# Kernel tuning notes

Hardware: AMD Instinct MI355X
Metric: run time of the kernel (lower is better)

The kernel has to match this reference:

```python
import jax, jax.numpy as jnp
import numpy as np

N_HEAD = 16
ROPE_BASE = 10000.0
EPS = 1e-6


def _rms_norm(x):
    return x / jnp.sqrt(jnp.mean(x * x, axis=-1, keepdims=True) + EPS)


def _rotary_cos_sin(n_pos, dim, dtype):
    # NOTE: faithful to the source, n_pos == n_head (not seq_len) because
    # Rotary.forward reads x.shape[2] of a (B,T,H,D) tensor.
    inv_freq = 1.0 / (ROPE_BASE ** (jnp.arange(0, dim, 2, dtype=jnp.float32) / dim))
    t = jnp.arange(n_pos, dtype=jnp.float32)
    freqs = jnp.outer(t, inv_freq)  # (n_pos, dim//2)
    return jnp.cos(freqs).astype(dtype)[None, None], jnp.sin(freqs).astype(dtype)[None, None]


def _apply_rotary(x, cos, sin):
    d = x.shape[-1] // 2
    x1, x2 = x[..., :d], x[..., d:]
    return jnp.concatenate([x1 * cos + x2 * sin, -x1 * sin + x2 * cos], axis=-1)


def setup_inputs() -> dict:
    key = jax.random.key(0)
    ks = jax.random.split(key, 8)
    B, T, C = 4, 1024, 2048
    x = jax.random.normal(ks[0], (B, T, C), dtype=jnp.float32)
    v1 = jax.random.normal(ks[1], (B, T, N_HEAD, C // N_HEAD), dtype=jnp.float32)
    s = 0.02
    W_qkv = jax.random.normal(ks[2], (C, 3 * C), dtype=jnp.float32) * s
    b_qkv = jax.random.normal(ks[3], (3 * C,), dtype=jnp.float32) * s
    W_proj = jax.random.normal(ks[4], (C, C), dtype=jnp.float32) * s
    b_proj = jax.random.normal(ks[5], (C,), dtype=jnp.float32) * s
    lamb = jnp.float32(0.5)
    return {"x": x, "v1": v1, "W_qkv": W_qkv, "b_qkv": b_qkv,
            "W_proj": W_proj, "b_proj": b_proj, "lamb": lamb}


def reference(x, v1, W_qkv, b_qkv, W_proj, b_proj, lamb):
    B, T, C = x.shape
    H = N_HEAD
    D = C // H
    qkv = x @ W_qkv + b_qkv  # (B,T,3C)
    q, k, v = jnp.split(qkv, 3, axis=-1)
    q = q.reshape(B, T, H, D)
    k = k.reshape(B, T, H, D)
    v = v.reshape(B, T, H, D)
    v1 = v1.reshape(B, T, H, D)
    value = (1.0 - lamb) * v + lamb * v1  # lambda value-residual mix
    q = _rms_norm(q)
    k = _rms_norm(k)
    cos, sin = _rotary_cos_sin(H, D, x.dtype)  # rotary over head axis (source bug, kept)
    q = _apply_rotary(q, cos, sin)
    k = _apply_rotary(k, cos, sin)
    # causal attention, default flex_attention scale 1/sqrt(D)
    scale = 1.0 / jnp.sqrt(jnp.float32(D)).astype(x.dtype)
    scores = jnp.einsum('bqhd,bkhd->bhqk', q, k) * scale
    causal = jnp.tril(jnp.ones((T, T), dtype=bool))
    scores = jnp.where(causal[None, None], scores, jnp.finfo(scores.dtype).min)
    probs = jax.nn.softmax(scores, axis=-1)
    attn = jnp.einsum('bhqk,bkhd->bqhd', probs, value).reshape(B, T, C)
    out = attn @ W_proj + b_proj
    return out, v1
```

## Files before the change

kernel.cpp:

```cpp
#include <hip/hip_runtime.h>
#include <stdint.h>
#include <stddef.h>

typedef unsigned short u16;
typedef __attribute__((ext_vector_type(8))) short  bf16x8;
typedef __attribute__((ext_vector_type(4))) unsigned short u16x4;
typedef __attribute__((ext_vector_type(4))) float  f32x4;

#define DEVI __device__ __forceinline__

DEVI float bf2f(u16 u){ union{uint32_t i; float f;} v; v.i = ((uint32_t)u)<<16; return v.f; }
DEVI u16 f2bf(float f){ union{float f; uint32_t i;} v; v.f=f; uint32_t r = v.i + 0x7fffu + ((v.i>>16)&1u); return (u16)(r>>16); }

DEVI void gload_lds16(const void* g, void* l){
  __builtin_amdgcn_global_load_lds((const __attribute__((address_space(1))) void*)g,
                                   (__attribute__((address_space(3))) void*)l, 16, 0, 0);
}

__global__ __launch_bounds__(256) void k_prep(
    const float* __restrict__ x,     u16* __restrict__ xb,
    const float* __restrict__ Wqkv,  u16* __restrict__ WqkvT,
    const float* __restrict__ Wproj, u16* __restrict__ WprojT)
{
  __shared__ float tile[32][33];
  int bid = blockIdx.x;
  int tid = threadIdx.x;
  if (bid < 2048){
    int i = (bid*256 + tid)*4;
    const int st = 2048*256*4;
    for (; i < 8388608; i += st){
      f32x4 v = *(const f32x4*)(x + i);
      u16x4 o;
      #pragma unroll
      for (int j=0;j<4;j++) o[j] = f2bf(v[j]);
      *(u16x4*)(xb + i) = o;
    }
    return;
  }
  const float* in; u16* out; int K, N, nb, kb;
  if (bid < 2048 + 12288){
    int b2 = bid - 2048; in = Wqkv; out = WqkvT; K = 2048; N = 6144;
    nb = (b2 % 192)*32; kb = (b2 / 192)*32;
  } else {
    int b3 = bid - 2048 - 12288; in = Wproj; out = WprojT; K = 2048; N = 2048;
    nb = (b3 % 64)*32; kb = (b3 / 64)*32;
  }
  int tx = tid & 31, ty = tid >> 5;
  #pragma unroll
  for (int i=0;i<32;i+=8)
    tile[ty+i][tx] = in[(size_t)(kb+ty+i)*N + nb+tx];
  __syncthreads();
  #pragma unroll
  for (int i=0;i<32;i+=8)
    out[(size_t)(nb+ty+i)*K + kb+tx] = f2bf(tile[tx][ty+i]);
}

#define STG_A(SLAB, GSRC) \
  gload_lds16((GSRC) + off0, (SLAB) + tid*8);
#define STG_B(SLAB, GSRC) \
  gload_lds16((GSRC) + off0, (SLAB) + tid*8); \
  gload_lds16((GSRC) + off1, (SLAB) + 4096 + tid*8);

#define RD4(SLAB, ROWBASE, DST) \
  { _Pragma("unroll") for (int f=0; f<4; f++){ \
      int row_ = (ROWBASE) + f*16 + lr; \
      int rp_ = row_>>1; \
      int slot_ = ((((row_&1)<<2) | lg) ^ (rp_&7)); \
      DST[f] = *(const bf16x8*)((const char*)(SLAB) + rp_*128 + slot_*16); } }

#define MM16(AA, BB) \
  __builtin_amdgcn_s_setprio(1); \
  { _Pragma("unroll") for (int f=0; f<4; f++) \
    { _Pragma("unroll") for (int nf=0; nf<4; nf++) \
      acc[f][nf] = __builtin_amdgcn_mfma_f32_16x16x32_bf16(AA[f], BB[nf], acc[f][nf], 0,0,0); } } \
  __builtin_amdgcn_s_setprio(0);

#define BAR_LGKM \
  __builtin_amdgcn_s_barrier(); \
  __builtin_amdgcn_sched_barrier(0); \
  asm volatile("s_waitcnt lgkmcnt(0)" ::: "memory"); \
  __builtin_amdgcn_sched_barrier(0);

#define WAITV(N) asm volatile("s_waitcnt vmcnt(" #N ")" ::: "memory");
#define ORDER_FENCE __builtin_amdgcn_sched_barrier(0); asm volatile("" ::: "memory");

template<bool OUT_BF16>
__global__ __launch_bounds__(512) void k_gemm128x256(
    const u16* __restrict__ A, const u16* __restrict__ Bt,
    const float* __restrict__ bias, void* __restrict__ Cout,
    int M, int N, int K, int nbnx)
{
  __shared__ __attribute__((aligned(16))) u16 sA[3][2][4096];
  __shared__ __attribute__((aligned(16))) u16 sB[3][2][8192];
  int orig = blockIdx.x;
  int xcd = orig & 7;
  int idx = orig >> 3;
  int bnx = idx % nbnx;
  int bm  = idx / nbnx;
  int bn  = xcd*nbnx + bnx;
  const int tid = threadIdx.x;
  const int wid = tid>>6, l = tid&63;
  const int lr = l&15, lg = l>>4;
  const int wm = wid>>2, wn = wid&3;
  const int rba = wm*64, rbb = wn*64;

  uint32_t off0, off1;
  { int cc=tid;     int rp=cc>>3, cb=(cc&7)^(rp&7); off0 = (uint32_t)((rp*2+(cb>>2))*K + (cb&3)*8); }
  { int cc=512+tid; int rp=cc>>3, cb=(cc&7)^(rp&7); off1 = (uint32_t)((rp*2+(cb>>2))*K + (cb&3)*8); }
  const u16* Ab = A + (size_t)bm*128*K;
  const u16* Bb = Bt + (size_t)bn*256*K;

  f32x4 acc[4][4] = {};
  bf16x8 a0[4], a1[4], b0[4], b1[4];
  const int NT = K>>6;

  STG_B(&sB[0][0][0], Bb);      STG_A(&sA[0][0][0], Ab);      ORDER_FENCE;
  STG_B(&sB[0][1][0], Bb+32);   STG_A(&sA[0][1][0], Ab+32);   ORDER_FENCE;
  STG_B(&sB[1][0][0], Bb+64);   STG_A(&sA[1][0][0], Ab+64);
  WAITV(6);
  __builtin_amdgcn_s_barrier();
  __builtin_amdgcn_sched_barrier(0);

  int s0=0, s1=1, s2=2;
  for (int t=0; t<=NT-3; ++t){
    const u16* A1 = Ab + (t+1)*64;  const u16* B1 = Bb + (t+1)*64;
    const u16* A2 = Ab + (t+2)*64;  const u16* B2 = Bb + (t+2)*64;
    RD4(&sB[s0][0][0], rbb, b0); RD4(&sA[s0][0][0], rba, a0);
    STG_B(&sB[s1][1][0], B1+32); STG_A(&sA[s1][1][0], A1+32);
    WAITV(6);
    BAR_LGKM; MM16(a0, b0);
    RD4(&sB[s0][1][0], rbb, b1); RD4(&sA[s0][1][0], rba, a1);
    STG_B(&sB[s2][0][0], B2);    STG_A(&sA[s2][0][0], A2);
    WAITV(6);
    BAR_LGKM; MM16(a1, b1);
    int tmp=s0; s0=s1; s1=s2; s2=tmp;
  }
  {
    const u16* A1 = Ab + (NT-1)*64;  const u16* B1 = Bb + (NT-1)*64;
    RD4(&sB[s0][0][0], rbb, b0); RD4(&sA[s0][0][0], rba, a0);
    STG_B(&sB[s1][1][0], B1+32); STG_A(&sA[s1][1][0], A1+32);
    WAITV(6);
    BAR_LGKM; MM16(a0, b0);
    RD4(&sB[s0][1][0], rbb, b1); RD4(&sA[s0][1][0], rba, a1);
    WAITV(3);
    BAR_LGKM; MM16(a1, b1);
  }
  {
    RD4(&sB[s1][0][0], rbb, b0); RD4(&sA[s1][0][0], rba, a0);
    WAITV(0);
    BAR_LGKM; MM16(a0, b0);
    RD4(&sB[s1][1][0], rbb, b1); RD4(&sA[s1][1][0], rba, a1);
    BAR_LGKM; MM16(a1, b1);
  }

  #pragma unroll
  for (int nf=0; nf<4; nf++){
    int col = bn*256 + wn*64 + nf*16 + lr;
    float bv = bias[col];
    #pragma unroll
    for (int m=0; m<4; m++){
      #pragma unroll
      for (int j=0; j<4; j++){
        int row = bm*128 + wm*64 + m*16 + lg*4 + j;
        float v = acc[m][nf][j] + bv;
        if (OUT_BF16) ((u16*)Cout)[(size_t)row*N + col] = f2bf(v);
        else          ((float*)Cout)[(size_t)row*N + col] = v;
      }
    }
  }
}

template<bool OUT_BF16>
__global__ __launch_bounds__(256) void k_gemm_bt(
    const u16* __restrict__ A, const u16* __restrict__ Bt,
    const float* __restrict__ bias, void* __restrict__ Cout,
    int M, int N, int K, int nbnx)
{
  __shared__ __attribute__((aligned(16))) u16 sA[128*64];
  __shared__ __attribute__((aligned(16))) u16 sB[128*64];
  int orig = blockIdx.x;
  int xcd = orig & 7;
  int idx = orig >> 3;
  int bn  = xcd*nbnx + idx % nbnx;
  int bm  = idx / nbnx;
  const int tid = threadIdx.x;
  const int w = tid>>6, l = tid&63;
  const int lr = l&15, lg = l>>4;
  const int wr = (w>>1)*64, wc = (w&1)*64;
  const size_t rowA = (size_t)bm*128;
  const size_t rowB = (size_t)bn*128;
  f32x4 acc[4][4] = {};
  for (int k0=0; k0<K; k0+=64){
    #pragma unroll
    for (int it=0; it<4; ++it){
      int c = it*256 + tid;
      int r = c>>3, k8 = (c&7) ^ (r&7);
      gload_lds16(A + (rowA+r)*K + k0 + k8*8, &sA[c*8]);
    }
    #pragma unroll
    for (int it=0; it<4; ++it){
      int c = it*256 + tid;
      int r = c>>3, k8 = (c&7) ^ (r&7);
      gload_lds16(Bt + (rowB+r)*K + k0 + k8*8, &sB[c*8]);
    }
    __syncthreads();
    #pragma unroll
    for (int ks=0; ks<2; ++ks){
      bf16x8 af[4], bfr[4];
      #pragma unroll
      for (int m=0;m<4;m++){
        int row = wr + m*16 + lr, k = ks*32 + lg*8;
        int byt = ((row<<7) + (k<<1)) ^ ((row&7)<<4);
        af[m] = *(const bf16x8*)((const char*)sA + byt);
      }
      #pragma unroll
      for (int n=0;n<4;n++){
        int row = wc + n*16 + lr, k = ks*32 + lg*8;
        int byt = ((row<<7) + (k<<1)) ^ ((row&7)<<4);
        bfr[n] = *(const bf16x8*)((const char*)sB + byt);
      }
      #pragma unroll
      for (int m=0;m<4;m++)
        #pragma unroll
        for (int n=0;n<4;n++)
          acc[m][n] = __builtin_amdgcn_mfma_f32_16x16x32_bf16(af[m], bfr[n], acc[m][n], 0,0,0);
    }
    __syncthreads();
  }
  #pragma unroll
  for (int n=0;n<4;n++){
    int col = bn*128 + wc + n*16 + lr;
    float bv = bias[col];
    #pragma unroll
    for (int m=0;m<4;m++){
      #pragma unroll
      for (int j=0;j<4;j++){
        int row = bm*128 + wr + m*16 + lg*4 + j;
        float v = acc[m][n][j] + bv;
        if (OUT_BF16) ((u16*)Cout)[(size_t)row*N + col] = f2bf(v);
        else          ((float*)Cout)[(size_t)row*N + col] = v;
      }
    }
  }
}

DEVI void unpack16(const u16* p, float* f){
  bf16x8 a = *(const bf16x8*)p, b = *(const bf16x8*)(p+8);
  #pragma unroll
  for (int i=0;i<8;i++){ f[i]=bf2f((u16)a[i]); f[8+i]=bf2f((u16)b[i]); }
}

__global__ __launch_bounds__(256) void k_qkv_post(
    const u16*  __restrict__ qkv,
    const float* __restrict__ v1,
    const float* __restrict__ lambp,
    u16* __restrict__ qn,
    u16* __restrict__ kn,
    u16* __restrict__ vT,
    float* __restrict__ v1out)
{
  __shared__ float cosv[64], sinv[64];
  __shared__ __attribute__((aligned(16))) u16 sv[64][136];
  int bid = blockIdx.x;
  int tb = bid & 15, h = (bid>>4)&15, b = bid>>8;
  int tid = threadIdx.x;
  if (tid < 64){
    float ang = (float)h * exp2f(-(float)tid * 0.2076205059304595f);
    cosv[tid] = cosf(ang);
    sinv[tid] = sinf(ang);
  }
  float lamb = lambp[0];
  int row = tid>>2, p = tid&3;
  int t = tb*64 + row;
  size_t base = ((size_t)(b*1024 + t))*6144 + (size_t)h*128;
  __syncthreads();

  #pragma unroll
  for (int qc=0; qc<2; ++qc){
    const u16* src = qkv + base + qc*2048;
    u16* dst = (qc==0 ? qn : kn) + ((size_t)(b*1024+t))*2048 + h*128;
    int j0 = p*16;
    float x1[16], x2[16];
    unpack16(src + j0, x1);
    unpack16(src + 64 + j0, x2);
    float ss = 0.f;
    #pragma unroll
    for (int i=0;i<16;i++) ss += x1[i]*x1[i] + x2[i]*x2[i];
    ss += __shfl_xor(ss, 1);
    ss += __shfl_xor(ss, 2);
    float rn = rsqrtf(ss*(1.0f/128.0f) + 1e-6f);
    bf16x8 o1a,o1b,o2a,o2b;
    #pragma unroll
    for (int i=0;i<16;i++){
      float c = cosv[j0+i], s = sinv[j0+i];
      u16 a = f2bf(( x1[i]*c + x2[i]*s)*rn);
      u16 bq= f2bf((-x1[i]*s + x2[i]*c)*rn);
      if (i<8){ o1a[i]=(short)a; o2a[i]=(short)bq; } else { o1b[i-8]=(short)a; o2b[i-8]=(short)bq; }
    }
    *(bf16x8*)(dst + j0)      = o1a;
    *(bf16x8*)(dst + j0 + 8)  = o1b;
    *(bf16x8*)(dst + 64 + j0)     = o2a;
    *(bf16x8*)(dst + 64 + j0 + 8) = o2b;
  }

  {
    const u16* srcv = qkv + base + 4096;
    size_t v1off = (((size_t)(b*1024+t))*16 + h)*128;
    const float* src1 = v1 + v1off;
    float* dst1 = v1out + v1off;
    int d0 = p*32;
    #pragma unroll
    for (int c8=0;c8<4;c8++){
      bf16x8 vv = *(const bf16x8*)(srcv + d0 + c8*8);
      f32x4 a0 = *(const f32x4*)(src1 + d0 + c8*8);
      f32x4 a1 = *(const f32x4*)(src1 + d0 + c8*8 + 4);
      *(f32x4*)(dst1 + d0 + c8*8) = a0;
      *(f32x4*)(dst1 + d0 + c8*8 + 4) = a1;
      bf16x8 o;
      #pragma unroll
      for (int i=0;i<8;i++){
        float x1v = (i<4)? a0[i] : a1[i-4];
        o[i] = (short)f2bf((1.0f-lamb)*bf2f((u16)vv[i]) + lamb*x1v);
      }
      *(bf16x8*)(&sv[row][d0 + c8*8]) = o;
    }
  }
  __syncthreads();
  {
    int d = tid>>1, tc = (tid&1)*32;
    u16 tmp[32];
    #pragma unroll
    for (int i=0;i<32;i++) tmp[i] = sv[tc+i][d];
    u16* dst = vT + (((size_t)(b*16+h))*128 + d)*1024 + tb*64 + tc;
    #pragma unroll
    for (int c8=0;c8<4;c8++){
      bf16x8 o;
      #pragma unroll
      for (int i=0;i<8;i++) o[i]=(short)tmp[c8*8+i];
      *(bf16x8*)(dst + c8*8) = o;
    }
  }
}

__global__ __launch_bounds__(256) void k_attn(
    const u16* __restrict__ Q,
    const u16* __restrict__ Kn,
    const u16* __restrict__ Vt,
    u16* __restrict__ O)
{
  __shared__ __attribute__((aligned(16))) u16 sK[2][64*128];
  __shared__ __attribute__((aligned(16))) u16 sV[2][128*64];
  __shared__ __attribute__((aligned(16))) u16 sP[4][16*64];
  int bid = blockIdx.x;
  int qi = 15 - (bid>>6);
  int bh = bid & 63;
  int h = bh & 15, b = bh >> 4;
  int tid = threadIdx.x, w = tid>>6, l = tid&63, lr = l&15, lg = l>>4;
  int qrow = qi*64 + w*16;
  bf16x8 aq[4];
  {
    const u16* qp = Q + ((size_t)(b*1024 + qrow + lr))*2048 + h*128 + lg*8;
    #pragma unroll
    for (int ks=0; ks<4; ++ks) aq[ks] = *(const bf16x8*)(qp + ks*32);
  }
  f32x4 accO[8] = {};
  float mrun[4], srun[4];
  #pragma unroll
  for (int j=0;j<4;j++){ mrun[j] = -INFINITY; srun[j]=0.f; }
  const float scale = 0.08838834764831845f;
  const size_t kbase = (size_t)(b*1024)*2048 + (size_t)h*128;
  const u16* vbase = Vt + ((size_t)(b*16+h))*128*1024;

  auto STAGE = [&](int kt, int buf){
    #pragma unroll
    for (int it=0; it<4; ++it){
      int c = it*256+tid;
      int key = c>>4, d16 = (c&15)^(key&7);
      gload_lds16(Kn + kbase + (size_t)(kt*64+key)*2048 + d16*8, &sK[buf][c*8]);
    }
    #pragma unroll
    for (int it=0; it<4; ++it){
      int c = it*256+tid;
      int d = c>>3, k8 = (c&7)^(d&7);
      gload_lds16(vbase + (size_t)d*1024 + kt*64 + k8*8, &sV[buf][c*8]);
    }
  };

  STAGE(0, 0);
  int cur = 0;
  for (int kt=0; kt<=qi; ++kt){
    if (kt < qi){
      STAGE(kt+1, cur^1);
      asm volatile("s_waitcnt vmcnt(8)" ::: "memory");
    } else {
      asm volatile("s_waitcnt vmcnt(0)" ::: "memory");
    }
    __builtin_amdgcn_s_barrier();
    __builtin_amdgcn_sched_barrier(0);
    const char* kb = (const char*)sK[cur];
    const char* vb = (const char*)sV[cur];

    f32x4 accS[4] = {};
    __builtin_amdgcn_s_setprio(1);
    #pragma unroll
    for (int ks=0; ks<4; ++ks){
      #pragma unroll
      for (int n=0;n<4;n++){
        int key = n*16+lr, k = ks*32+lg*8;
        int byt = ((key<<8) + (k<<1)) ^ ((key&7)<<4);
        bf16x8 bk = *(const bf16x8*)(kb + byt);
        accS[n] = __builtin_amdgcn_mfma_f32_16x16x32_bf16(aq[ks], bk, accS[n], 0,0,0);
      }
    }
    __builtin_amdgcn_s_setprio(0);
    bool diag = (kt == qi);
    float pj[4][4];
    #pragma unroll
    for (int j=0;j<4;j++){
      int qg = qrow + lg*4 + j;
      float mx = -INFINITY;
      #pragma unroll
      for (int n=0;n<4;n++){
        float s = accS[n][j]*scale;
        if (diag && (kt*64 + n*16 + lr) > qg) s = -1e30f;
        pj[n][j] = s;
        mx = fmaxf(mx, s);
      }
      #pragma unroll
      for (int off=1; off<16; off<<=1) mx = fmaxf(mx, __shfl_xor(mx, off));
      float mnew = fmaxf(mrun[j], mx);
      float fac = __expf(mrun[j] - mnew);
      float ps = 0.f;
      #pragma unroll
      for (int n=0;n<4;n++){ float e = __expf(pj[n][j]-mnew); pj[n][j]=e; ps += e; }
      #pragma unroll
      for (int off=1; off<16; off<<=1) ps += __shfl_xor(ps, off);
      srun[j] = srun[j]*fac + ps;
      mrun[j] = mnew;
      #pragma unroll
      for (int n=0;n<8;n++) accO[n][j] *= fac;
    }
    #pragma unroll
    for (int n=0;n<4;n++)
      #pragma unroll
      for (int j=0;j<4;j++){
        int q = lg*4+j, key = n*16+lr;
        int byt = ((q<<7) + (key<<1)) ^ ((q&7)<<4);
        *(u16*)((char*)sP[w] + byt) = f2bf(pj[n][j]);
      }
    bf16x8 pA[2];
    #pragma unroll
    for (int ks=0; ks<2; ++ks){
      int k = ks*32 + lg*8;
      int byt = ((lr<<7) + (k<<1)) ^ ((lr&7)<<4);
      pA[ks] = *(const bf16x8*)((const char*)sP[w] + byt);
    }
    __builtin_amdgcn_s_setprio(1);
    #pragma unroll
    for (int ks=0; ks<2; ++ks)
      #pragma unroll
      for (int n=0;n<8;n++){
        int d = n*16+lr, k = ks*32+lg*8;
        int byt = ((d<<7) + (k<<1)) ^ ((d&7)<<4);
        bf16x8 bv = *(const bf16x8*)(vb + byt);
        accO[n] = __builtin_amdgcn_mfma_f32_16x16x32_bf16(pA[ks], bv, accO[n], 0,0,0);
      }
    __builtin_amdgcn_s_setprio(0);
    __builtin_amdgcn_s_barrier();
    cur ^= 1;
  }
  #pragma unroll
  for (int j=0;j<4;j++){
    float inv = 1.0f / srun[j];
    int row = qrow + lg*4 + j;
    u16* op = O + ((size_t)(b*1024+row))*2048 + h*128;
    #pragma unroll
    for (int n=0;n<8;n++)
      op[n*16+lr] = f2bf(accO[n][j]*inv);
  }
}

extern "C" void kernel_launch(void* const* d_in, const int* in_sizes, int n_in,
                              void* d_out, int out_size, void* d_ws, size_t ws_size,
                              hipStream_t stream)
{
  const float* x     = (const float*)d_in[0];
  const float* v1    = (const float*)d_in[1];
  const float* Wqkv  = (const float*)d_in[2];
  const float* bqkv  = (const float*)d_in[3];
  const float* Wproj = (const float*)d_in[4];
  const float* bproj = (const float*)d_in[5];
  const float* lamb  = (const float*)d_in[6];

  char* ws = (char*)d_ws;
  u16* qkv_b  = (u16*)(ws);
  u16* WqkvT  = (u16*)(ws +  50331648);
  u16* WprojT = (u16*)(ws +  75497472);
  u16* xb     = (u16*)(ws +  83886080);
  u16* vT     = xb;
  u16* qn     = (u16*)(ws + 100663296);
  u16* kn     = (u16*)(ws + 117440512);
  u16* attn_b = qkv_b;

  float* out = (float*)d_out;

  hipLaunchKernelGGL(k_prep, dim3(2048+12288+4096), dim3(256), 0, stream,
                     x, xb, Wqkv, WqkvT, Wproj, WprojT);
  hipLaunchKernelGGL((k_gemm128x256<true>),  dim3(768), dim3(512), 0, stream, xb, WqkvT, bqkv, (void*)qkv_b, 4096, 6144, 2048, 3);
  hipLaunchKernelGGL(k_qkv_post, dim3(1024), dim3(256), 0, stream, qkv_b, v1, lamb, qn, kn, vT, out + 8388608);
  hipLaunchKernelGGL(k_attn, dim3(1024), dim3(256), 0, stream, qn, kn, vT, attn_b);
  hipLaunchKernelGGL((k_gemm_bt<false>), dim3(512), dim3(256), 0, stream, attn_b, WprojT, bproj, (void*)out, 4096, 2048, 2048, 2);
}
```

Measured before the change: 274.9 us.

## Enlarge QKV GEMM tile to 256x256 with double-buffered quadrant-scheduled pipeline

Replaces the 128x256 QKV projection GEMM with a 256x256 tile per 512-thread block, using two LDS buffers instead of three and issuing MFMAs in four quadrants interleaved with async global-to-LDS loads. Each wave now holds an 8x4 accumulator grid, which doubles reuse of every loaded A/B fragment and halves the block count to 384. The aim is to cut LDS and global traffic per FLOP. In exchange, register pressure is higher (launch bounds limit to one block per CU), the grid of 384 may leave CUs unevenly loaded on a 256-CU part, and the schedule needs many more barriers.

```diff
diff --git a/kernel.cpp b/kernel.cpp
--- a/kernel.cpp
+++ b/kernel.cpp
@@ -55,116 +55,133 @@
     out[(size_t)(nb+ty+i)*K + kb+tx] = f2bf(tile[tx][ty+i]);
 }
 
-#define STG_A(SLAB, GSRC) \
-  gload_lds16((GSRC) + off0, (SLAB) + tid*8);
-#define STG_B(SLAB, GSRC) \
-  gload_lds16((GSRC) + off0, (SLAB) + tid*8); \
-  gload_lds16((GSRC) + off1, (SLAB) + 4096 + tid*8);
-
-#define RD4(SLAB, ROWBASE, DST) \
-  { _Pragma("unroll") for (int f=0; f<4; f++){ \
-      int row_ = (ROWBASE) + f*16 + lr; \
-      int rp_ = row_>>1; \
-      int slot_ = ((((row_&1)<<2) | lg) ^ (rp_&7)); \
-      DST[f] = *(const bf16x8*)((const char*)(SLAB) + rp_*128 + slot_*16); } }
-
-#define MM16(AA, BB) \
+#define STG(SLABP, GHALF) \
+  gload_lds16((GHALF) + offG[0], (SLABP) + tid*8); \
+  gload_lds16((GHALF) + offG[1], (SLABP) + 4096 + tid*8);
+
+#define RD_A(BUF, MH) \
+  { const char* sp_ = (const char*)&sA[BUF][wm][0]; \
+    _Pragma("unroll") for (int f=0; f<4; f++) \
+    _Pragma("unroll") for (int ks=0; ks<2; ks++){ \
+      int r_ = (MH)*64 + f*16 + lr; \
+      int k16_ = ks*4 + lg; \
+      a[f*2+ks] = *(const bf16x8*)(sp_ + r_*128 + ((k16_ ^ (r_&7))<<4)); } }
+
+#define RD_B(BUF, NH, BREG) \
+  { const char* sp_ = (const char*)&sB[BUF][wn>>1][0]; \
+    _Pragma("unroll") for (int g=0; g<2; g++) \
+    _Pragma("unroll") for (int ks=0; ks<2; ks++){ \
+      int r_ = (wn&1)*64 + (NH)*32 + g*16 + lr; \
+      int k16_ = ks*4 + lg; \
+      BREG[g*2+ks] = *(const bf16x8*)(sp_ + r_*128 + ((k16_ ^ (r_&7))<<4)); } }
+
+#define MMQ(MH, NH, BREG) \
   __builtin_amdgcn_s_setprio(1); \
   { _Pragma("unroll") for (int f=0; f<4; f++) \
-    { _Pragma("unroll") for (int nf=0; nf<4; nf++) \
-      acc[f][nf] = __builtin_amdgcn_mfma_f32_16x16x32_bf16(AA[f], BB[nf], acc[f][nf], 0,0,0); } } \
+    _Pragma("unroll") for (int g=0; g<2; g++) \
+    _Pragma("unroll") for (int ks=0; ks<2; ks++) \
+      acc[(MH)*4+f][(NH)*2+g] = __builtin_amdgcn_mfma_f32_16x16x32_bf16( \
+        a[f*2+ks], BREG[g*2+ks], acc[(MH)*4+f][(NH)*2+g], 0,0,0); } \
   __builtin_amdgcn_s_setprio(0);
 
-#define BAR_LGKM \
+#define BARX \
   __builtin_amdgcn_s_barrier(); \
-  __builtin_amdgcn_sched_barrier(0); \
   asm volatile("s_waitcnt lgkmcnt(0)" ::: "memory"); \
   __builtin_amdgcn_sched_barrier(0);
 
+#define BAR2 \
+  __builtin_amdgcn_s_barrier(); \
+  __builtin_amdgcn_sched_barrier(0);
+
 #define WAITV(N) asm volatile("s_waitcnt vmcnt(" #N ")" ::: "memory");
 #define ORDER_FENCE __builtin_amdgcn_sched_barrier(0); asm volatile("" ::: "memory");
 
 template<bool OUT_BF16>
-__global__ __launch_bounds__(512) void k_gemm128x256(
+__global__ __launch_bounds__(512, 1) void k_gemm256m(
     const u16* __restrict__ A, const u16* __restrict__ Bt,
     const float* __restrict__ bias, void* __restrict__ Cout,
     int M, int N, int K, int nbnx)
 {
-  __shared__ __attribute__((aligned(16))) u16 sA[3][2][4096];
-  __shared__ __attribute__((aligned(16))) u16 sB[3][2][8192];
+  __shared__ __attribute__((aligned(16))) u16 sA[2][2][8192];
+  __shared__ __attribute__((aligned(16))) u16 sB[2][2][8192];
   int orig = blockIdx.x;
   int xcd = orig & 7;
   int idx = orig >> 3;
-  int bnx = idx % nbnx;
+  int bn  = xcd*nbnx + idx % nbnx;
   int bm  = idx / nbnx;
-  int bn  = xcd*nbnx + bnx;
   const int tid = threadIdx.x;
   const int wid = tid>>6, l = tid&63;
   const int lr = l&15, lg = l>>4;
   const int wm = wid>>2, wn = wid&3;
-  const int rba = wm*64, rbb = wn*64;
-
-  uint32_t off0, off1;
-  { int cc=tid;     int rp=cc>>3, cb=(cc&7)^(rp&7); off0 = (uint32_t)((rp*2+(cb>>2))*K + (cb&3)*8); }
-  { int cc=512+tid; int rp=cc>>3, cb=(cc&7)^(rp&7); off1 = (uint32_t)((rp*2+(cb>>2))*K + (cb&3)*8); }
-  const u16* Ab = A + (size_t)bm*128*K;
-  const u16* Bb = Bt + (size_t)bn*256*K;
-
-  f32x4 acc[4][4] = {};
-  bf16x8 a0[4], a1[4], b0[4], b1[4];
-  const int NT = K>>6;
-
-  STG_B(&sB[0][0][0], Bb);      STG_A(&sA[0][0][0], Ab);      ORDER_FENCE;
-  STG_B(&sB[0][1][0], Bb+32);   STG_A(&sA[0][1][0], Ab+32);   ORDER_FENCE;
-  STG_B(&sB[1][0][0], Bb+64);   STG_A(&sA[1][0][0], Ab+64);
-  WAITV(6);
+
+  uint32_t offG[2];
+  #pragma unroll
+  for (int j=0;j<2;j++){
+    int s = tid + 512*j;
+    int r = s>>3, kg = (s&7)^(r&7);
+    offG[j] = (uint32_t)(r*K + kg*8);
+  }
+  const u16* Abase = A + (size_t)(bm*256)*K;
+  const u16* Bbase = Bt + (size_t)(bn*256)*K;
+  const size_t HK = (size_t)128*K;
+
+  f32x4 acc[8][4] = {};
+  bf16x8 a[8], b0[4], b1[4];
+  const int NI = K>>7;
+
+  STG(&sA[0][0][0], Abase);
+  STG(&sA[0][1][0], Abase + HK);
+  ORDER_FENCE;
+  STG(&sB[0][0][0], Bbase);
+  STG(&sB[0][1][0], Bbase + HK);
+  ORDER_FENCE;
+  STG(&sB[1][0][0], Bbase + 64);
+  STG(&sB[1][1][0], Bbase + HK + 64);
+  WAITV(4);
   __builtin_amdgcn_s_barrier();
   __builtin_amdgcn_sched_barrier(0);
 
-  int s0=0, s1=1, s2=2;
-  for (int t=0; t<=NT-3; ++t){
-    const u16* A1 = Ab + (t+1)*64;  const u16* B1 = Bb + (t+1)*64;
-    const u16* A2 = Ab + (t+2)*64;  const u16* B2 = Bb + (t+2)*64;
-    RD4(&sB[s0][0][0], rbb, b0); RD4(&sA[s0][0][0], rba, a0);
-    STG_B(&sB[s1][1][0], B1+32); STG_A(&sA[s1][1][0], A1+32);
-    WAITV(6);
-    BAR_LGKM; MM16(a0, b0);
-    RD4(&sB[s0][1][0], rbb, b1); RD4(&sA[s0][1][0], rba, a1);
-    STG_B(&sB[s2][0][0], B2);    STG_A(&sA[s2][0][0], A2);
-    WAITV(6);
-    BAR_LGKM; MM16(a1, b1);
-    int tmp=s0; s0=s1; s1=s2; s2=tmp;
-  }
-  {
-    const u16* A1 = Ab + (NT-1)*64;  const u16* B1 = Bb + (NT-1)*64;
-    RD4(&sB[s0][0][0], rbb, b0); RD4(&sA[s0][0][0], rba, a0);
-    STG_B(&sB[s1][1][0], B1+32); STG_A(&sA[s1][1][0], A1+32);
-    WAITV(6);
-    BAR_LGKM; MM16(a0, b0);
-    RD4(&sB[s0][1][0], rbb, b1); RD4(&sA[s0][1][0], rba, a1);
-    WAITV(3);
-    BAR_LGKM; MM16(a1, b1);
-  }
-  {
-    RD4(&sB[s1][0][0], rbb, b0); RD4(&sA[s1][0][0], rba, a0);
-    WAITV(0);
-    BAR_LGKM; MM16(a0, b0);
-    RD4(&sB[s1][1][0], rbb, b1); RD4(&sA[s1][1][0], rba, a1);
-    BAR_LGKM; MM16(a1, b1);
+  for (int t=0; t<NI; ++t){
+    const bool full = (t+1 < NI);
+    const u16* Aq = Abase + (2*t+1)*64;
+    const u16* An = Abase + (2*t+2)*64;
+    const u16* Bn = Bbase + (2*t+2)*64;
+    RD_A(0,0); RD_B(0,0,b0);
+    STG(&sA[1][0][0], Aq);
+    BARX; MMQ(0,0,b0); BAR2;
+    RD_B(0,1,b1);
+    STG(&sA[1][1][0], Aq + HK);
+    BARX; MMQ(0,1,b1); BAR2;
+    RD_A(0,1);
+    if (full){ STG(&sB[0][0][0], Bn); }
+    BARX; MMQ(1,1,b1); BAR2;
+    if (full){ STG(&sB[0][1][0], Bn + HK); WAITV(4); } else { WAITV(0); }
+    BARX; MMQ(1,0,b0); BAR2;
+    RD_A(1,0); RD_B(1,0,b0);
+    if (full){ STG(&sA[0][0][0], An); }
+    BARX; MMQ(0,0,b0); BAR2;
+    RD_B(1,1,b1);
+    if (full){ STG(&sA[0][1][0], An + HK); }
+    BARX; MMQ(0,1,b1); BAR2;
+    RD_A(1,1);
+    if (full){ STG(&sB[1][0][0], Bn + 64); }
+    BARX; MMQ(1,1,b1); BAR2;
+    if (full){ STG(&sB[1][1][0], Bn + HK + 64); WAITV(4); }
+    BARX; MMQ(1,0,b0); BAR2;
   }
 
   #pragma unroll
   for (int nf=0; nf<4; nf++){
-    int col = bn*256 + wn*64 + nf*16 + lr;
+    int col = bn*256 + wn*64 + (nf>>1)*32 + (nf&1)*16 + lr;
     float bv = bias[col];
     #pragma unroll
-    for (int m=0; m<4; m++){
+    for (int mf=0; mf<8; mf++){
+      int rbase = bm*256 + wm*128 + (mf>>2)*64 + (mf&3)*16 + lg*4;
       #pragma unroll
       for (int j=0; j<4; j++){
-        int row = bm*128 + wm*64 + m*16 + lg*4 + j;
-        float v = acc[m][nf][j] + bv;
-        if (OUT_BF16) ((u16*)Cout)[(size_t)row*N + col] = f2bf(v);
-        else          ((float*)Cout)[(size_t)row*N + col] = v;
+        float v = acc[mf][nf][j] + bv;
+        if (OUT_BF16) ((u16*)Cout)[(size_t)(rbase+j)*N + col] = f2bf(v);
+        else          ((float*)Cout)[(size_t)(rbase+j)*N + col] = v;
       }
     }
   }
@@ -176,8 +193,8 @@
     const float* __restrict__ bias, void* __restrict__ Cout,
     int M, int N, int K, int nbnx)
 {
-  __shared__ __attribute__((aligned(16))) u16 sA[128*64];
-  __shared__ __attribute__((aligned(16))) u16 sB[128*64];
+  __shared__ __attribute__((aligned(16))) u16 sA2[128*64];
+  __shared__ __attribute__((aligned(16))) u16 sB2[128*64];
   int orig = blockIdx.x;
   int xcd = orig & 7;
   int idx = orig >> 3;
@@ -195,13 +212,13 @@
     for (int it=0; it<4; ++it){
       int c = it*256 + tid;
       int r = c>>3, k8 = (c&7) ^ (r&7);
-      gload_lds16(A + (rowA+r)*K + k0 + k8*8, &sA[c*8]);
+      gload_lds16(A + (rowA+r)*K + k0 + k8*8, &sA2[c*8]);
     }
     #pragma unroll
     for (int it=0; it<4; ++it){
       int c = it*256 + tid;
       int r = c>>3, k8 = (c&7) ^ (r&7);
-      gload_lds16(Bt + (rowB+r)*K + k0 + k8*8, &sB[c*8]);
+      gload_lds16(Bt + (rowB+r)*K + k0 + k8*8, &sB2[c*8]);
     }
     __syncthreads();
     #pragma unroll
@@ -211,13 +228,13 @@
       for (int m=0;m<4;m++){
         int row = wr + m*16 + lr, k = ks*32 + lg*8;
         int byt = ((row<<7) + (k<<1)) ^ ((row&7)<<4);
-        af[m] = *(const bf16x8*)((const char*)sA + byt);
+        af[m] = *(const bf16x8*)((const char*)sA2 + byt);
       }
       #pragma unroll
       for (int n=0;n<4;n++){
         int row = wc + n*16 + lr, k = ks*32 + lg*8;
         int byt = ((row<<7) + (k<<1)) ^ ((row&7)<<4);
-        bfr[n] = *(const bf16x8*)((const char*)sB + byt);
+        bfr[n] = *(const bf16x8*)((const char*)sB2 + byt);
       }
       #pragma unroll
       for (int m=0;m<4;m++)
@@ -506,7 +523,7 @@
 
   hipLaunchKernelGGL(k_prep, dim3(2048+12288+4096), dim3(256), 0, stream,
                      x, xb, Wqkv, WqkvT, Wproj, WprojT);
-  hipLaunchKernelGGL((k_gemm128x256<true>),  dim3(768), dim3(512), 0, stream, xb, WqkvT, bqkv, (void*)qkv_b, 4096, 6144, 2048, 3);
+  hipLaunchKernelGGL((k_gemm256m<true>),  dim3(384), dim3(512), 0, stream, xb, WqkvT, bqkv, (void*)qkv_b, 4096, 6144, 2048, 3);
   hipLaunchKernelGGL(k_qkv_post, dim3(1024), dim3(256), 0, stream, qkv_b, v1, lamb, qn, kn, vT, out + 8388608);
   hipLaunchKernelGGL(k_attn, dim3(1024), dim3(256), 0, stream, qn, kn, vT, attn_b);
   hipLaunchKernelGGL((k_gemm_bt<false>), dim3(512), dim3(256), 0, stream, attn_b, WprojT, bproj, (void*)out, 4096, 2048, 2048, 2);
```

Measured after the change: 286.8 us, median of 2. +4.3%, slower.
